# Optimization experiments

Measured on AMD Instinct MI355X. Metric: run time of the kernel, lower is better.

Reference implementation:

```python
import jax, jax.numpy as jnp
import numpy as np

EMBED_DIM = 256
HEADS = 8
HEAD_DIM = EMBED_DIM // HEADS
T = 8            # time grid points
N0, N1 = 32, 32  # spatial grid
MAX_PATCH = 16   # static slot budget per cell (last slot = grid latent token)
NEG = -1e30


def construct_grid():
    g0 = jnp.linspace(0.0, 1.0, N0)
    g1 = jnp.linspace(0.0, 1.0, N1)
    G0, G1 = jnp.meshgrid(g0, g1, indexing='ij')
    return jnp.stack([G0, G1], axis=-1)  # [N0, N1, 2]


def setup_inputs() -> dict:
    key = jax.random.key(0)
    ks = jax.random.split(key, 8)
    m, n = 4, 16384
    x = jax.random.uniform(ks[0], (m, n, 3))                       # coords: (time, s0, s1) in [0,1]
    z = jax.random.normal(ks[1], (m, n, EMBED_DIM))
    time_grid = jnp.tile(jnp.linspace(0.0, 1.0, T)[None], (m, 1))  # [m, T] uniform time grid
    latents = jax.random.normal(ks[2], (N0, N1, EMBED_DIM))
    grid = construct_grid()
    s = 1.0 / np.sqrt(EMBED_DIM)
    Wq = jax.random.normal(ks[3], (EMBED_DIM, EMBED_DIM)) * s
    Wk = jax.random.normal(ks[4], (EMBED_DIM, EMBED_DIM)) * s
    Wv = jax.random.normal(ks[5], (EMBED_DIM, EMBED_DIM)) * s
    Wo = jax.random.normal(ks[6], (EMBED_DIM, EMBED_DIM)) * s
    return {'x': x, 'z': z, 'time_grid': time_grid, 'latents': latents,
            'grid': grid, 'Wq': Wq, 'Wk': Wk, 'Wv': Wv, 'Wo': Wo}


def _cumcount(idx):
    # idx: [n] int; returns per-element count of prior occurrences of the same value
    n = idx.shape[0]
    order = jnp.argsort(idx)                 # stable
    srt = idx[order]
    ar = jnp.arange(n)
    is_start = jnp.concatenate([jnp.array([True]), srt[1:] != srt[:-1]])
    seg_start = jax.lax.cummax(jnp.where(is_start, ar, 0), axis=0)
    cc = ar - seg_start
    return jnp.zeros_like(idx).at[order].set(cc.astype(idx.dtype))


def _forward(x, z, time_grid, latents, grid, Wq, Wk, Wv, Wo):
    m, n, _ = x.shape
    t = time_grid.shape[1]
    S = t * N0 * N1
    # --- build x_grid: repeat spatial grid over (m,t), insert time coord at dim 0 ---
    xg_sp = jnp.broadcast_to(grid[None, None], (m, t, N0, N1, 2))
    tg = jnp.broadcast_to(time_grid[:, :, None, None, None], (m, t, N0, N1, 1))
    x_grid = jnp.concatenate([tg, xg_sp], axis=-1)          # [m,t,N0,N1,3]
    # --- nearest gridded neighbour (k=1): per-dim rounding on the regular grid ---
    grid_shape = jnp.array([t, N0, N1], jnp.float32)
    xg_flat = x_grid.reshape(m, S, 3)
    xmin = xg_flat.min(axis=1)                               # [m,3]
    xmax = xg_flat.max(axis=1)
    spacing = (xmax - xmin) / (grid_shape - 1.0)             # [m,3]
    multi = jnp.floor((x - xmin[:, None] + spacing[:, None] / 2) / spacing[:, None])
    multi = jnp.clip(multi, 0.0, grid_shape - 1.0)
    strides = jnp.array([N0 * N1, N1, 1], jnp.float32)
    nearest = jnp.sum(multi * strides, axis=-1).astype(jnp.int32)  # [m,n] flat cell id
    # --- per-cell slot allocation via cumulative count ---
    cum = jax.vmap(_cumcount)(nearest)                       # [m,n]
    P = MAX_PATCH
    valid = cum < (P - 1)                                    # last slot reserved for grid token
    bidx = jnp.arange(m)[:, None]
    cell = jnp.where(valid, nearest, S)                      # out-of-bounds -> dropped
    slot = jnp.minimum(cum, P - 2)
    # --- scatter points into the joint grid [m, S, P, E]; slot P-1 = grid latent ---
    joint = jnp.zeros((m, S, P, EMBED_DIM), z.dtype)
    joint = joint.at[bidx, cell, slot].set(z, mode='drop')
    z_grid_flat = jnp.broadcast_to(
        latents.reshape(1, 1, N0 * N1, EMBED_DIM), (m, t, N0 * N1, EMBED_DIM)
    ).reshape(m, S, EMBED_DIM)
    joint = joint.at[:, :, P - 1].set(z_grid_flat)
    counts = jnp.zeros((m, S), jnp.int32).at[bidx, cell].add(1, mode='drop')
    counts = jnp.minimum(counts, P - 1)
    att_mask = jnp.concatenate(
        [jnp.arange(P - 1)[None, None] < counts[..., None],
         jnp.ones((m, S, 1), bool)], axis=-1)                # [m,S,P]
    # --- masked multi-head cross attention: 1 query (grid latent) per cell ---
    q = (z_grid_flat @ Wq).reshape(m, S, HEADS, HEAD_DIM)
    k = (joint @ Wk).reshape(m, S, P, HEADS, HEAD_DIM)
    v = (joint @ Wv).reshape(m, S, P, HEADS, HEAD_DIM)
    logits = jnp.einsum('mshd,msphd->mshp', q, k) / np.sqrt(HEAD_DIM)
    logits = jnp.where(att_mask[:, :, None, :], logits, NEG)
    attn = jax.nn.softmax(logits, axis=-1)
    out = jnp.einsum('mshp,msphd->mshd', attn, v).reshape(m, S, EMBED_DIM) @ Wo
    z_grid = out.reshape(m, t, N0, N1, EMBED_DIM)
    return x_grid, z_grid


def reference(x, z, time_grid, latents, grid, Wq, Wk, Wv, Wo):
    return _forward(x, z, time_grid, latents, grid, Wq, Wk, Wv, Wo)
```

## Files before the change

### kernel.cpp

```cpp
#include <hip/hip_runtime.h>
#include <hip/hip_bf16.h>

#define T_ 8
#define N0_ 32
#define N1_ 32
#define SP_ (N0_*N1_)
#define S_ (T_*SP_)
#define E_ 256
#define P_ 16
#define NH_ 8
#define HD_ 32

typedef __attribute__((ext_vector_type(8))) short short8;
typedef __attribute__((ext_vector_type(4))) float f32x4;
typedef __attribute__((ext_vector_type(8))) unsigned short u16x8;

__device__ __forceinline__ unsigned short f2bf(float f) {
  __hip_bfloat16 h = __float2bfloat16(f);
  return *reinterpret_cast<unsigned short*>(&h);
}
__device__ __forceinline__ float bf2f(unsigned short u) {
  return __uint_as_float((unsigned)u << 16);
}

__device__ __forceinline__ void gl_lds16(const void* g, void* l) {
  __builtin_amdgcn_global_load_lds(
      (const __attribute__((address_space(1))) unsigned int*)(g),
      (__attribute__((address_space(3))) unsigned int*)(l), 16, 0, 0);
}

__global__ __launch_bounds__(256) void prep(const float* __restrict__ x,
                                            const float* __restrict__ tg,
                                            const float* __restrict__ grid,
                                            float* __restrict__ out,
                                            int* __restrict__ counts,
                                            int* __restrict__ cell_raw,
                                            const float* __restrict__ Wq,
                                            const float* __restrict__ Wk,
                                            const float* __restrict__ Wv,
                                            const float* __restrict__ Wo,
                                            unsigned short* __restrict__ wT,
                                            int m, int n, int tot_xg) {
  __shared__ float ts[64][65];
  __shared__ float st[4][6];
  int bid = blockIdx.x;
  int tid = threadIdx.x;
  if (bid < 256) {
    if (tid < 64) {
      float mn0 = 1e30f, mx0 = -1e30f, mn1 = 1e30f, mx1 = -1e30f;
      for (int i = tid; i < SP_; i += 64) {
        float g0 = grid[i*2], g1 = grid[i*2+1];
        mn0 = fminf(mn0, g0); mx0 = fmaxf(mx0, g0);
        mn1 = fminf(mn1, g1); mx1 = fmaxf(mx1, g1);
      }
      for (int msk = 32; msk; msk >>= 1) {
        mn0 = fminf(mn0, __shfl_xor(mn0, msk));
        mx0 = fmaxf(mx0, __shfl_xor(mx0, msk));
        mn1 = fminf(mn1, __shfl_xor(mn1, msk));
        mx1 = fmaxf(mx1, __shfl_xor(mx1, msk));
      }
      if (tid == 0) {
        for (int b = 0; b < m; ++b) {
          float tmn = 1e30f, tmx = -1e30f;
          for (int tt = 0; tt < T_; ++tt) {
            float v = tg[b*T_ + tt];
            tmn = fminf(tmn, v); tmx = fmaxf(tmx, v);
          }
          st[b][0] = tmn; st[b][1] = mn0; st[b][2] = mn1;
          st[b][3] = (tmx - tmn) / (float)(T_ - 1);
          st[b][4] = (mx0 - mn0) / (float)(N0_ - 1);
          st[b][5] = (mx1 - mn1) / (float)(N1_ - 1);
        }
      }
    }
    __syncthreads();
    int idx = bid * 256 + tid;
    if (idx < tot_xg) {
      int sp = idx & (SP_ - 1);
      int bt = idx >> 10;
      out[idx*3 + 0] = tg[bt];
      out[idx*3 + 1] = grid[sp*2 + 0];
      out[idx*3 + 2] = grid[sp*2 + 1];
    }
    if (idx < m*n) {
      int b = idx / n;
      int j = idx - b*n;
      const float* s = st[b];
      float xt = x[(size_t)idx*3 + 0], x0 = x[(size_t)idx*3 + 1], x1 = x[(size_t)idx*3 + 2];
      float m0 = floorf((xt - s[0] + s[3]*0.5f) / s[3]);
      float m1 = floorf((x0 - s[1] + s[4]*0.5f) / s[4]);
      float m2 = floorf((x1 - s[2] + s[5]*0.5f) / s[5]);
      m0 = fminf(fmaxf(m0, 0.f), (float)(T_ - 1));
      m1 = fminf(fmaxf(m1, 0.f), (float)(N0_ - 1));
      m2 = fminf(fmaxf(m2, 0.f), (float)(N1_ - 1));
      int sc = (int)m0 * SP_ + (int)m1 * N1_ + (int)m2;
      int cg = b * S_ + sc;
      int old = atomicAdd(&counts[cg], 1);
      if (old < P_) cell_raw[(size_t)cg * P_ + old] = j;
    }
    return;
  }
  int wb = bid - 256;
  int mat = wb >> 4;
  int tile = wb & 15;
  int tr = (tile >> 2) * 64;
  int tc = (tile & 3) * 64;
  const float* W = mat == 0 ? Wq : mat == 1 ? Wk : mat == 2 ? Wv : Wo;
  int r = tid >> 2, c0 = (tid & 3) * 16;
#pragma unroll
  for (int i = 0; i < 4; ++i) {
    float4 v = *(const float4*)&W[(size_t)(tr + r) * 256 + tc + c0 + i*4];
    ts[r][c0 + i*4 + 0] = v.x; ts[r][c0 + i*4 + 1] = v.y;
    ts[r][c0 + i*4 + 2] = v.z; ts[r][c0 + i*4 + 3] = v.w;
  }
  __syncthreads();
  u16x8 o0, o1;
#pragma unroll
  for (int i = 0; i < 8; ++i) o0[i] = f2bf(ts[c0 + i][r]);
#pragma unroll
  for (int i = 0; i < 8; ++i) o1[i] = f2bf(ts[c0 + 8 + i][r]);
  unsigned short* dst = wT + (size_t)(mat * 256 + tc + r) * 256 + tr + c0;
  *(u16x8*)dst = o0;
  *(u16x8*)(dst + 8) = o1;
}

template <typename OutT>
__device__ __forceinline__ void f32a_body(char* __restrict__ ldsbuf,
                                          const float* __restrict__ A,
                                          const unsigned short* __restrict__ BT,
                                          OutT* __restrict__ C,
                                          int CP, int ldc, int L, int tid) {
  float* As = (float*)ldsbuf;
  unsigned short* Bs = (unsigned short*)(ldsbuf + 32768);
  int rp = L / CP, cp = L - rp * CP;

  int wid = tid >> 6, lane = tid & 63, l15 = lane & 15, slot = lane >> 4;
  int wr = (wid >> 1) * 64, wc = (wid & 1) * 64;

  int arl = lane >> 4, aG = lane & 15;
  int brl = lane >> 3, bG = lane & 7;

  f32x4 acc[4][4] = {};

#pragma unroll
  for (int kt = 0; kt < 4; ++kt) {
#pragma unroll
    for (int d = 0; d < 8; ++d) {
      int row = wid * 32 + d * 4 + arl;
      const float* src = A + (size_t)(rp * 128 + row) * 256 + kt * 64
                         + (size_t)((aG ^ (row & 15)) << 2);
      gl_lds16(src, As + (wid * 32 + d * 4) * 64);
    }
#pragma unroll
    for (int d = 0; d < 4; ++d) {
      int row = wid * 32 + d * 8 + brl;
      const unsigned short* src = BT + (size_t)(cp * 128 + row) * 256 + kt * 64
                                  + (size_t)((bG ^ (row & 7)) << 3);
      gl_lds16(src, Bs + (wid * 32 + d * 8) * 64);
    }
    asm volatile("s_waitcnt vmcnt(0)" ::: "memory");
    __builtin_amdgcn_s_barrier();
    asm volatile("" ::: "memory");
#pragma unroll
    for (int kf = 0; kf < 2; ++kf) {
      short8 afr[4], bfr[4];
      int kg = kf * 4 + slot;
#pragma unroll
      for (int mm = 0; mm < 4; ++mm) {
        int row = wr + mm * 16 + l15;
        f32x4 a0 = *(const f32x4*)&As[row * 64 + (((2 * kg    ) ^ l15) << 2)];
        f32x4 a1 = *(const f32x4*)&As[row * 64 + (((2 * kg + 1) ^ l15) << 2)];
        short8 af;
        af[0]=f2bf(a0[0]); af[1]=f2bf(a0[1]); af[2]=f2bf(a0[2]); af[3]=f2bf(a0[3]);
        af[4]=f2bf(a1[0]); af[5]=f2bf(a1[1]); af[6]=f2bf(a1[2]); af[7]=f2bf(a1[3]);
        afr[mm] = af;
      }
#pragma unroll
      for (int nn = 0; nn < 4; ++nn) {
        int col = wc + nn * 16 + l15;
        bfr[nn] = *(const short8*)&Bs[col * 64 + ((kg ^ (l15 & 7)) << 3)];
      }
#pragma unroll
      for (int mm = 0; mm < 4; ++mm)
#pragma unroll
        for (int nn = 0; nn < 4; ++nn)
          acc[mm][nn] = __builtin_amdgcn_mfma_f32_16x16x32_bf16(afr[mm], bfr[nn], acc[mm][nn], 0, 0, 0);
    }
    asm volatile("" ::: "memory");
    __builtin_amdgcn_s_barrier();
    asm volatile("" ::: "memory");
  }

#pragma unroll
  for (int mm = 0; mm < 4; ++mm) {
#pragma unroll
    for (int nn = 0; nn < 4; ++nn) {
      int grow0 = rp * 128 + wr + mm * 16 + slot * 4;
      int gcol  = cp * 128 + wc + nn * 16 + l15;
#pragma unroll
      for (int j = 0; j < 4; ++j) {
        size_t o = (size_t)(grow0 + j) * ldc + gcol;
        if constexpr (__is_same(OutT, float)) C[o] = acc[mm][nn][j];
        else                                  C[o] = __float2bfloat16(acc[mm][nn][j]);
      }
    }
  }
}

template <typename OutT>
__device__ __forceinline__ void g2l_body(unsigned short* __restrict__ ldsbuf,
                                         const unsigned short* __restrict__ A,
                                         const unsigned short* __restrict__ BT,
                                         OutT* __restrict__ C,
                                         int CP, int ldc, int L, int tid) {
  int rp = L / CP, cp = L - rp * CP;

  int wid = tid >> 6, lane = tid & 63, l15 = lane & 15, slot = lane >> 4;
  int wr = (wid >> 1) * 64, wc = (wid & 1) * 64;

  int r8 = lane >> 3, k8 = lane & 7;
  int colsw = (k8 ^ r8) << 3;
  const unsigned short* ga0 = A  + (size_t)(rp * 128 + wid * 32 + r8) * 256 + colsw;
  const unsigned short* gb0 = BT + (size_t)(cp * 128 + wid * 32 + r8) * 256 + colsw;
  unsigned short* As = ldsbuf;
  unsigned short* Bs = ldsbuf + 8192;

  f32x4 acc[4][4] = {};

#pragma unroll
  for (int kt = 0; kt < 4; ++kt) {
    const unsigned short* ga = ga0 + kt * 64;
    const unsigned short* gb = gb0 + kt * 64;
    gl_lds16(ga,          As + (wid*32     ) * 64);
    gl_lds16(ga +  8*256, As + (wid*32 +  8) * 64);
    gl_lds16(ga + 16*256, As + (wid*32 + 16) * 64);
    gl_lds16(ga + 24*256, As + (wid*32 + 24) * 64);
    gl_lds16(gb,          Bs + (wid*32     ) * 64);
    gl_lds16(gb +  8*256, Bs + (wid*32 +  8) * 64);
    gl_lds16(gb + 16*256, Bs + (wid*32 + 16) * 64);
    gl_lds16(gb + 24*256, Bs + (wid*32 + 24) * 64);
    asm volatile("s_waitcnt vmcnt(0)" ::: "memory");
    __builtin_amdgcn_s_barrier();
    asm volatile("" ::: "memory");
#pragma unroll
    for (int kf = 0; kf < 2; ++kf) {
      short8 afr[4], bfr[4];
      int sx = (kf * 4 + slot) ^ (l15 & 7);
#pragma unroll
      for (int mm = 0; mm < 4; ++mm) {
        int row = wr + mm * 16 + l15;
        afr[mm] = *(const short8*)&As[row * 64 + (sx << 3)];
      }
#pragma unroll
      for (int nn = 0; nn < 4; ++nn) {
        int col = wc + nn * 16 + l15;
        bfr[nn] = *(const short8*)&Bs[col * 64 + (sx << 3)];
      }
#pragma unroll
      for (int mm = 0; mm < 4; ++mm)
#pragma unroll
        for (int nn = 0; nn < 4; ++nn)
          acc[mm][nn] = __builtin_amdgcn_mfma_f32_16x16x32_bf16(afr[mm], bfr[nn], acc[mm][nn], 0, 0, 0);
    }
    asm volatile("" ::: "memory");
    __builtin_amdgcn_s_barrier();
    asm volatile("" ::: "memory");
  }

#pragma unroll
  for (int mm = 0; mm < 4; ++mm) {
#pragma unroll
    for (int nn = 0; nn < 4; ++nn) {
      int grow0 = rp * 128 + wr + mm * 16 + slot * 4;
      int gcol  = cp * 128 + wc + nn * 16 + l15;
#pragma unroll
      for (int j = 0; j < 4; ++j) {
        size_t o = (size_t)(grow0 + j) * ldc + gcol;
        if constexpr (__is_same(OutT, float)) C[o] = acc[mm][nn][j];
        else                                  C[o] = __float2bfloat16(acc[mm][nn][j]);
      }
    }
  }
}

__global__ __launch_bounds__(256, 3) void phase2(const float* __restrict__ z,
                                                 const unsigned short* __restrict__ wT,
                                                 __hip_bfloat16* __restrict__ kv,
                                                 const float* __restrict__ latents,
                                                 float* __restrict__ lat,
                                                 const int* __restrict__ counts,
                                                 int* __restrict__ cell_raw,
                                                 int* __restrict__ pts2, int total) {
  __shared__ char lds[49152];
  int bid = blockIdx.x;
  if (bid < 2048) {
    int L = (bid & 7) * 256 + (bid >> 3);
    f32a_body<__hip_bfloat16>(lds, z, wT + (size_t)256*256, kv, 4, 512, L, threadIdx.x);
    return;
  }
  if (bid < 2096) {
    f32a_body<float>(lds, latents, wT, lat, 6, 768, bid - 2048, threadIdx.x);
    return;
  }
  int cg = (bid - 2096) * 256 + threadIdx.x;
  if (cg >= total) return;
  int cnt = counts[cg];
  int stored = cnt < P_ ? cnt : P_;
  int eff = cnt < (P_ - 1) ? cnt : (P_ - 1);
  int* p = cell_raw + (size_t)cg * P_;
  for (int i = 1; i < stored; ++i) {
    int key = p[i]; int j = i - 1;
    while (j >= 0 && p[j] > key) { p[j+1] = p[j]; --j; }
    p[j+1] = key;
  }
  int* o = pts2 + (size_t)cg * P_;
  o[0] = eff;
  for (int i = 0; i < eff; ++i) o[1 + i] = p[i];
}

template <typename OutT>
__global__ __launch_bounds__(256, 3) void gemm_g2l(const unsigned short* __restrict__ A,
                                                   const unsigned short* __restrict__ BT,
                                                   OutT* __restrict__ C,
                                                   int CP, int ldc) {
  __shared__ unsigned short lds[2 * 128 * 64];
  int nb = gridDim.x, bid = blockIdx.x;
  int L = bid;
  if ((nb & 7) == 0) L = (bid & 7) * (nb >> 3) + (bid >> 3);
  g2l_body<OutT>(lds, A, BT, C, CP, ldc, L, threadIdx.x);
}

__global__ __launch_bounds__(256) void attn_kernel(
    const float* __restrict__ lat,
    const __hip_bfloat16* __restrict__ kv,
    const int* __restrict__ pts2,
    __hip_bfloat16* __restrict__ attn_out, int n) {
  const float scale = 0.17677669529663687f;
  int wid = threadIdx.x >> 6;
  int lane = threadIdx.x & 63;
  int cellg = blockIdx.x * 4 + wid;
  int b = cellg >> 13;
  int c = cellg & (SP_ - 1);
  int d0 = lane << 2;

  const int* pp = pts2 + (size_t)cellg * P_;
  int4 h0 = *(const int4*)pp;
  int eff = h0.x;

  const float* latc = lat + c * 768 + d0;
  float4 q  = *(const float4*)latc;
  float4 kl = *(const float4*)(latc + 256);
  float4 vl = *(const float4*)(latc + 512);

  float p15 = q.x*kl.x + q.y*kl.y + q.z*kl.z + q.w*kl.w;
  p15 += __shfl_xor(p15, 1);
  p15 += __shfl_xor(p15, 2);
  p15 += __shfl_xor(p15, 4);
  float e15 = __expf(p15 * scale);
  float ssum = e15;
  float4 acc;
  acc.x = e15 * vl.x; acc.y = e15 * vl.y; acc.z = e15 * vl.z; acc.w = e15 * vl.w;

  const unsigned short* kvp = (const unsigned short*)kv;
  size_t bbase = (size_t)b * n;

  int pt[4]; pt[0] = h0.y; pt[1] = h0.z; pt[2] = h0.w; pt[3] = 0;
  int done = 0, cap = 3;
  while (done < eff) {
    int np = eff - done; if (np > cap) np = cap;
    ushort4 kr[4], vr[4];
#pragma unroll
    for (int i = 0; i < 4; ++i) if (i < np) {
      size_t row = (bbase + (size_t)pt[i]) * 512;
      kr[i] = *(const ushort4*)(kvp + row + d0);
      vr[i] = *(const ushort4*)(kvp + row + 256 + d0);
    }
    float e[4];
#pragma unroll
    for (int i = 0; i < 4; ++i) if (i < np) {
      float p = q.x*bf2f(kr[i].x) + q.y*bf2f(kr[i].y) + q.z*bf2f(kr[i].z) + q.w*bf2f(kr[i].w);
      p += __shfl_xor(p, 1);
      p += __shfl_xor(p, 2);
      p += __shfl_xor(p, 4);
      e[i] = __expf(p * scale);
    }
#pragma unroll
    for (int i = 0; i < 4; ++i) if (i < np) {
      ssum += e[i];
      acc.x += e[i] * bf2f(vr[i].x);
      acc.y += e[i] * bf2f(vr[i].y);
      acc.z += e[i] * bf2f(vr[i].z);
      acc.w += e[i] * bf2f(vr[i].w);
    }
    done += np;
    cap = 4;
    if (done < eff) {
      int4 h = *(const int4*)(pp + 1 + done);
      pt[0] = h.x; pt[1] = h.y; pt[2] = h.z; pt[3] = h.w;
    }
  }
  float inv = 1.f / ssum;
  ushort4 o;
  o.x = f2bf(acc.x * inv); o.y = f2bf(acc.y * inv);
  o.z = f2bf(acc.z * inv); o.w = f2bf(acc.w * inv);
  *(ushort4*)((unsigned short*)attn_out + (size_t)cellg * E_ + d0) = o;
}

extern "C" void kernel_launch(void* const* d_in, const int* in_sizes, int n_in,
                              void* d_out, int out_size, void* d_ws, size_t ws_size,
                              hipStream_t stream) {
  const float* x       = (const float*)d_in[0];
  const float* z       = (const float*)d_in[1];
  const float* tg      = (const float*)d_in[2];
  const float* latents = (const float*)d_in[3];
  const float* grid    = (const float*)d_in[4];
  const float* Wq      = (const float*)d_in[5];
  const float* Wk      = (const float*)d_in[6];
  const float* Wv      = (const float*)d_in[7];
  const float* Wo      = (const float*)d_in[8];

  int m = in_sizes[2] / T_;
  int n = in_sizes[1] / (m * E_);
  int MS = m * S_;
  float* out = (float*)d_out;
  int tot_xg = m * T_ * SP_;

  char* w = (char*)d_ws;
  auto alloc = [&](size_t bytes) { char* p = w; w += (bytes + 255) & ~(size_t)255; return p; };
  int*   counts     = (int*)  alloc((size_t)MS * 4);
  int*   cell_raw   = (int*)  alloc((size_t)MS * P_ * 4);
  int*   pts2       = (int*)  alloc((size_t)MS * P_ * 4);
  unsigned short* wT = (unsigned short*)alloc((size_t)1024 * 256 * 2);
  float* lat        = (float*)alloc((size_t)SP_ * 768 * 4);
  __hip_bfloat16* kv       = (__hip_bfloat16*)alloc((size_t)m * n * 512 * 2);
  __hip_bfloat16* attn_out = (__hip_bfloat16*)alloc((size_t)MS * E_ * 2);

  (void)hipMemsetAsync(counts, 0, (size_t)MS * 4, stream);

  prep<<<320, 256, 0, stream>>>(x, tg, grid, out, counts, cell_raw,
                                Wq, Wk, Wv, Wo, wT, m, n, tot_xg);

  phase2<<<2224, 256, 0, stream>>>(z, wT, kv, latents, lat, counts, cell_raw, pts2, MS);

  attn_kernel<<<MS/4, 256, 0, stream>>>(lat, kv, pts2, attn_out, n);

  gemm_g2l<float><<<512, 256, 0, stream>>>(
      (const unsigned short*)attn_out, wT + (size_t)768*256, out + (size_t)tot_xg * 3, 2, 256);
}
```

Measured before the change: 83.46 us.

## Defer V projection past attention and fuse V/O projections into attention kernel

Only K is projected for all points now. The attention kernel accumulates softmax-weighted raw z rows per head and applies Wv afterwards on the per-cell mixed vectors, since attn·(zWv) = (attn·z)Wv. The V and Wo projections are then done with MFMA inside the same kernel, which removes the separate output GEMM and the attn_out round trip. This halves the large point projection GEMM and the kv buffer. In exchange it adds per-head fp32 z gathers, eight heads of accumulator registers per lane, and small per-block GEMMs whose weights are read straight from global memory.

```diff
diff --git a/kernel.cpp b/kernel.cpp
--- a/kernel.cpp
+++ b/kernel.cpp
@@ -207,85 +207,9 @@
   }
 }
 
-template <typename OutT>
-__device__ __forceinline__ void g2l_body(unsigned short* __restrict__ ldsbuf,
-                                         const unsigned short* __restrict__ A,
-                                         const unsigned short* __restrict__ BT,
-                                         OutT* __restrict__ C,
-                                         int CP, int ldc, int L, int tid) {
-  int rp = L / CP, cp = L - rp * CP;
-
-  int wid = tid >> 6, lane = tid & 63, l15 = lane & 15, slot = lane >> 4;
-  int wr = (wid >> 1) * 64, wc = (wid & 1) * 64;
-
-  int r8 = lane >> 3, k8 = lane & 7;
-  int colsw = (k8 ^ r8) << 3;
-  const unsigned short* ga0 = A  + (size_t)(rp * 128 + wid * 32 + r8) * 256 + colsw;
-  const unsigned short* gb0 = BT + (size_t)(cp * 128 + wid * 32 + r8) * 256 + colsw;
-  unsigned short* As = ldsbuf;
-  unsigned short* Bs = ldsbuf + 8192;
-
-  f32x4 acc[4][4] = {};
-
-#pragma unroll
-  for (int kt = 0; kt < 4; ++kt) {
-    const unsigned short* ga = ga0 + kt * 64;
-    const unsigned short* gb = gb0 + kt * 64;
-    gl_lds16(ga,          As + (wid*32     ) * 64);
-    gl_lds16(ga +  8*256, As + (wid*32 +  8) * 64);
-    gl_lds16(ga + 16*256, As + (wid*32 + 16) * 64);
-    gl_lds16(ga + 24*256, As + (wid*32 + 24) * 64);
-    gl_lds16(gb,          Bs + (wid*32     ) * 64);
-    gl_lds16(gb +  8*256, Bs + (wid*32 +  8) * 64);
-    gl_lds16(gb + 16*256, Bs + (wid*32 + 16) * 64);
-    gl_lds16(gb + 24*256, Bs + (wid*32 + 24) * 64);
-    asm volatile("s_waitcnt vmcnt(0)" ::: "memory");
-    __builtin_amdgcn_s_barrier();
-    asm volatile("" ::: "memory");
-#pragma unroll
-    for (int kf = 0; kf < 2; ++kf) {
-      short8 afr[4], bfr[4];
-      int sx = (kf * 4 + slot) ^ (l15 & 7);
-#pragma unroll
-      for (int mm = 0; mm < 4; ++mm) {
-        int row = wr + mm * 16 + l15;
-        afr[mm] = *(const short8*)&As[row * 64 + (sx << 3)];
-      }
-#pragma unroll
-      for (int nn = 0; nn < 4; ++nn) {
-        int col = wc + nn * 16 + l15;
-        bfr[nn] = *(const short8*)&Bs[col * 64 + (sx << 3)];
-      }
-#pragma unroll
-      for (int mm = 0; mm < 4; ++mm)
-#pragma unroll
-        for (int nn = 0; nn < 4; ++nn)
-          acc[mm][nn] = __builtin_amdgcn_mfma_f32_16x16x32_bf16(afr[mm], bfr[nn], acc[mm][nn], 0, 0, 0);
-    }
-    asm volatile("" ::: "memory");
-    __builtin_amdgcn_s_barrier();
-    asm volatile("" ::: "memory");
-  }
-
-#pragma unroll
-  for (int mm = 0; mm < 4; ++mm) {
-#pragma unroll
-    for (int nn = 0; nn < 4; ++nn) {
-      int grow0 = rp * 128 + wr + mm * 16 + slot * 4;
-      int gcol  = cp * 128 + wc + nn * 16 + l15;
-#pragma unroll
-      for (int j = 0; j < 4; ++j) {
-        size_t o = (size_t)(grow0 + j) * ldc + gcol;
-        if constexpr (__is_same(OutT, float)) C[o] = acc[mm][nn][j];
-        else                                  C[o] = __float2bfloat16(acc[mm][nn][j]);
-      }
-    }
-  }
-}
-
 __global__ __launch_bounds__(256, 3) void phase2(const float* __restrict__ z,
                                                  const unsigned short* __restrict__ wT,
-                                                 __hip_bfloat16* __restrict__ kv,
+                                                 __hip_bfloat16* __restrict__ k16,
                                                  const float* __restrict__ latents,
                                                  float* __restrict__ lat,
                                                  const int* __restrict__ counts,
@@ -293,16 +217,16 @@
                                                  int* __restrict__ pts2, int total) {
   __shared__ char lds[49152];
   int bid = blockIdx.x;
-  if (bid < 2048) {
-    int L = (bid & 7) * 256 + (bid >> 3);
-    f32a_body<__hip_bfloat16>(lds, z, wT + (size_t)256*256, kv, 4, 512, L, threadIdx.x);
+  if (bid < 1024) {
+    int L = (bid & 7) * 128 + (bid >> 3);
+    f32a_body<__hip_bfloat16>(lds, z, wT + (size_t)256*256, k16, 2, 256, L, threadIdx.x);
     return;
   }
-  if (bid < 2096) {
-    f32a_body<float>(lds, latents, wT, lat, 6, 768, bid - 2048, threadIdx.x);
+  if (bid < 1072) {
+    f32a_body<float>(lds, latents, wT, lat, 6, 768, bid - 1024, threadIdx.x);
     return;
   }
-  int cg = (bid - 2096) * 256 + threadIdx.x;
+  int cg = (bid - 1072) * 256 + threadIdx.x;
   if (cg >= total) return;
   int cnt = counts[cg];
   int stored = cnt < P_ ? cnt : P_;
@@ -318,92 +242,139 @@
   for (int i = 0; i < eff; ++i) o[1 + i] = p[i];
 }
 
-template <typename OutT>
-__global__ __launch_bounds__(256, 3) void gemm_g2l(const unsigned short* __restrict__ A,
-                                                   const unsigned short* __restrict__ BT,
-                                                   OutT* __restrict__ C,
-                                                   int CP, int ldc) {
-  __shared__ unsigned short lds[2 * 128 * 64];
-  int nb = gridDim.x, bid = blockIdx.x;
-  int L = bid;
-  if ((nb & 7) == 0) L = (bid & 7) * (nb >> 3) + (bid >> 3);
-  g2l_body<OutT>(lds, A, BT, C, CP, ldc, L, threadIdx.x);
-}
-
-__global__ __launch_bounds__(256) void attn_kernel(
-    const float* __restrict__ lat,
-    const __hip_bfloat16* __restrict__ kv,
-    const int* __restrict__ pts2,
-    __hip_bfloat16* __restrict__ attn_out, int n) {
+__global__ __launch_bounds__(256, 2) void mega_attn(const float* __restrict__ z,
+                                                    const float* __restrict__ latents,
+                                                    const float* __restrict__ lat,
+                                                    const __hip_bfloat16* __restrict__ k16,
+                                                    const unsigned short* __restrict__ wTv,
+                                                    const unsigned short* __restrict__ wTo,
+                                                    const int* __restrict__ pts2,
+                                                    float* __restrict__ outZ, int n) {
+  __shared__ unsigned short mixlds[16 * 2048];
+  __shared__ unsigned short avlds[16 * 256];
   const float scale = 0.17677669529663687f;
-  int wid = threadIdx.x >> 6;
-  int lane = threadIdx.x & 63;
-  int cellg = blockIdx.x * 4 + wid;
-  int b = cellg >> 13;
-  int c = cellg & (SP_ - 1);
+  int tid = threadIdx.x, w = tid >> 6, lane = tid & 63;
   int d0 = lane << 2;
-
-  const int* pp = pts2 + (size_t)cellg * P_;
-  int4 h0 = *(const int4*)pp;
-  int eff = h0.x;
-
-  const float* latc = lat + c * 768 + d0;
-  float4 q  = *(const float4*)latc;
-  float4 kl = *(const float4*)(latc + 256);
-  float4 vl = *(const float4*)(latc + 512);
-
-  float p15 = q.x*kl.x + q.y*kl.y + q.z*kl.z + q.w*kl.w;
-  p15 += __shfl_xor(p15, 1);
-  p15 += __shfl_xor(p15, 2);
-  p15 += __shfl_xor(p15, 4);
-  float e15 = __expf(p15 * scale);
-  float ssum = e15;
-  float4 acc;
-  acc.x = e15 * vl.x; acc.y = e15 * vl.y; acc.z = e15 * vl.z; acc.w = e15 * vl.w;
-
-  const unsigned short* kvp = (const unsigned short*)kv;
-  size_t bbase = (size_t)b * n;
-
-  int pt[4]; pt[0] = h0.y; pt[1] = h0.z; pt[2] = h0.w; pt[3] = 0;
-  int done = 0, cap = 3;
-  while (done < eff) {
-    int np = eff - done; if (np > cap) np = cap;
-    ushort4 kr[4], vr[4];
-#pragma unroll
-    for (int i = 0; i < 4; ++i) if (i < np) {
-      size_t row = (bbase + (size_t)pt[i]) * 512;
-      kr[i] = *(const ushort4*)(kvp + row + d0);
-      vr[i] = *(const ushort4*)(kvp + row + 256 + d0);
-    }
-    float e[4];
-#pragma unroll
-    for (int i = 0; i < 4; ++i) if (i < np) {
-      float p = q.x*bf2f(kr[i].x) + q.y*bf2f(kr[i].y) + q.z*bf2f(kr[i].z) + q.w*bf2f(kr[i].w);
-      p += __shfl_xor(p, 1);
-      p += __shfl_xor(p, 2);
-      p += __shfl_xor(p, 4);
-      e[i] = __expf(p * scale);
-    }
-#pragma unroll
-    for (int i = 0; i < 4; ++i) if (i < np) {
-      ssum += e[i];
-      acc.x += e[i] * bf2f(vr[i].x);
-      acc.y += e[i] * bf2f(vr[i].y);
-      acc.z += e[i] * bf2f(vr[i].z);
-      acc.w += e[i] * bf2f(vr[i].w);
-    }
-    done += np;
-    cap = 4;
-    if (done < eff) {
-      int4 h = *(const int4*)(pp + 1 + done);
-      pt[0] = h.x; pt[1] = h.y; pt[2] = h.z; pt[3] = h.w;
-    }
-  }
-  float inv = 1.f / ssum;
-  ushort4 o;
-  o.x = f2bf(acc.x * inv); o.y = f2bf(acc.y * inv);
-  o.z = f2bf(acc.z * inv); o.w = f2bf(acc.w * inv);
-  *(ushort4*)((unsigned short*)attn_out + (size_t)cellg * E_ + d0) = o;
+  int l7 = lane & 7;
+  int cg0 = blockIdx.x * 16;
+
+  for (int cc = 0; cc < 4; ++cc) {
+    int cellL = w * 4 + cc;
+    int cellg = cg0 + cellL;
+    int bidx = cellg >> 13;
+    int c = cellg & (SP_ - 1);
+
+    const float* latc = lat + c * 768 + d0;
+    float4 q  = *(const float4*)latc;
+    float4 kl = *(const float4*)(latc + 256);
+
+    const int* pp = pts2 + (size_t)cellg * P_;
+    int4 h0 = *(const int4*)pp;
+    int eff = h0.x;
+
+    float ss[8];
+    float mx[8][4];
+    {
+      float p = q.x*kl.x + q.y*kl.y + q.z*kl.z + q.w*kl.w;
+      p += __shfl_xor(p, 1); p += __shfl_xor(p, 2); p += __shfl_xor(p, 4);
+      float e = __expf(p * scale);
+      float4 zl = *(const float4*)(latents + (size_t)c * 256 + d0);
+#pragma unroll
+      for (int h = 0; h < 8; ++h) {
+        float eh = __shfl(e, (h << 3) | l7);
+        ss[h] = eh;
+        mx[h][0] = eh*zl.x; mx[h][1] = eh*zl.y; mx[h][2] = eh*zl.z; mx[h][3] = eh*zl.w;
+      }
+    }
+    size_t bb = (size_t)bidx * n;
+    const unsigned short* kp = (const unsigned short*)k16;
+    int pt[4]; pt[0] = h0.y; pt[1] = h0.z; pt[2] = h0.w; pt[3] = 0;
+    int done = 0, cap = 3;
+    while (done < eff) {
+      int np = eff - done; if (np > cap) np = cap;
+      ushort4 kr[4]; float4 zr[4];
+#pragma unroll
+      for (int i = 0; i < 4; ++i) if (i < np) {
+        size_t row = bb + (size_t)pt[i];
+        kr[i] = *(const ushort4*)(kp + row * 256 + d0);
+        zr[i] = *(const float4*)(z + row * 256 + d0);
+      }
+#pragma unroll
+      for (int i = 0; i < 4; ++i) if (i < np) {
+        float p = q.x*bf2f(kr[i].x) + q.y*bf2f(kr[i].y) + q.z*bf2f(kr[i].z) + q.w*bf2f(kr[i].w);
+        p += __shfl_xor(p, 1); p += __shfl_xor(p, 2); p += __shfl_xor(p, 4);
+        float e = __expf(p * scale);
+#pragma unroll
+        for (int h = 0; h < 8; ++h) {
+          float eh = __shfl(e, (h << 3) | l7);
+          ss[h] += eh;
+          mx[h][0] += eh*zr[i].x; mx[h][1] += eh*zr[i].y;
+          mx[h][2] += eh*zr[i].z; mx[h][3] += eh*zr[i].w;
+        }
+      }
+      done += np;
+      cap = 4;
+      if (done < eff) {
+        int4 hh = *(const int4*)(pp + 1 + done);
+        pt[0] = hh.x; pt[1] = hh.y; pt[2] = hh.z; pt[3] = hh.w;
+      }
+    }
+    unsigned base = (unsigned)cellL * 4096;
+    unsigned K = cellL & 7;
+#pragma unroll
+    for (int h = 0; h < 8; ++h) {
+      float inv = 1.f / ss[h];
+      unsigned g = (unsigned)(h * 32 + (lane >> 1));
+      unsigned addr = base + ((g ^ K) << 4) + ((unsigned)(d0 & 7) << 1);
+      ushort4 v;
+      v.x = f2bf(mx[h][0] * inv); v.y = f2bf(mx[h][1] * inv);
+      v.z = f2bf(mx[h][2] * inv); v.w = f2bf(mx[h][3] * inv);
+      *(ushort4*)((char*)mixlds + addr) = v;
+    }
+  }
+  __syncthreads();
+
+  int l15 = lane & 15, slot = lane >> 4;
+#pragma unroll
+  for (int hh = 0; hh < 2; ++hh) {
+    int h = w + hh * 4;
+    f32x4 acc0 = {}, acc1 = {};
+#pragma unroll
+    for (int ks = 0; ks < 8; ++ks) {
+      unsigned gA = (unsigned)(h * 32 + ks * 4 + slot);
+      short8 afr = *(const short8*)((const char*)mixlds + l15 * 4096 + ((gA ^ (unsigned)(l15 & 7)) << 4));
+      short8 b0 = *(const short8*)(wTv + (size_t)(h * 32 + l15) * 256 + ks * 32 + slot * 8);
+      short8 b1 = *(const short8*)(wTv + (size_t)(h * 32 + 16 + l15) * 256 + ks * 32 + slot * 8);
+      acc0 = __builtin_amdgcn_mfma_f32_16x16x32_bf16(afr, b0, acc0, 0, 0, 0);
+      acc1 = __builtin_amdgcn_mfma_f32_16x16x32_bf16(afr, b1, acc1, 0, 0, 0);
+    }
+#pragma unroll
+    for (int j = 0; j < 4; ++j) {
+      unsigned row = (unsigned)(slot * 4 + j);
+      unsigned c0 = (unsigned)(h * 32 + l15);
+      unsigned c1 = (unsigned)(h * 32 + 16 + l15);
+      *(unsigned short*)((char*)avlds + row * 512 + (((c0 >> 3) ^ row) << 4) + ((c0 & 7) << 1)) = f2bf(acc0[j]);
+      *(unsigned short*)((char*)avlds + row * 512 + (((c1 >> 3) ^ row) << 4) + ((c1 & 7) << 1)) = f2bf(acc1[j]);
+    }
+  }
+  __syncthreads();
+
+  f32x4 oacc[4] = {};
+#pragma unroll
+  for (int ks = 0; ks < 8; ++ks) {
+    unsigned gA = (unsigned)(ks * 4 + slot);
+    short8 afr = *(const short8*)((const char*)avlds + l15 * 512 + ((gA ^ (unsigned)l15) << 4));
+#pragma unroll
+    for (int nn = 0; nn < 4; ++nn) {
+      short8 bf = *(const short8*)(wTo + (size_t)(w * 64 + nn * 16 + l15) * 256 + ks * 32 + slot * 8);
+      oacc[nn] = __builtin_amdgcn_mfma_f32_16x16x32_bf16(afr, bf, oacc[nn], 0, 0, 0);
+    }
+  }
+#pragma unroll
+  for (int nn = 0; nn < 4; ++nn)
+#pragma unroll
+    for (int j = 0; j < 4; ++j)
+      outZ[(size_t)(cg0 + slot * 4 + j) * 256 + w * 64 + nn * 16 + l15] = oacc[nn][j];
 }
 
 extern "C" void kernel_launch(void* const* d_in, const int* in_sizes, int n_in,
@@ -432,18 +403,16 @@
   int*   pts2       = (int*)  alloc((size_t)MS * P_ * 4);
   unsigned short* wT = (unsigned short*)alloc((size_t)1024 * 256 * 2);
   float* lat        = (float*)alloc((size_t)SP_ * 768 * 4);
-  __hip_bfloat16* kv       = (__hip_bfloat16*)alloc((size_t)m * n * 512 * 2);
-  __hip_bfloat16* attn_out = (__hip_bfloat16*)alloc((size_t)MS * E_ * 2);
+  __hip_bfloat16* k16 = (__hip_bfloat16*)alloc((size_t)m * n * 256 * 2);
 
   (void)hipMemsetAsync(counts, 0, (size_t)MS * 4, stream);
 
   prep<<<320, 256, 0, stream>>>(x, tg, grid, out, counts, cell_raw,
                                 Wq, Wk, Wv, Wo, wT, m, n, tot_xg);
 
-  phase2<<<2224, 256, 0, stream>>>(z, wT, kv, latents, lat, counts, cell_raw, pts2, MS);
-
-  attn_kernel<<<MS/4, 256, 0, stream>>>(lat, kv, pts2, attn_out, n);
-
-  gemm_g2l<float><<<512, 256, 0, stream>>>(
-      (const unsigned short*)attn_out, wT + (size_t)768*256, out + (size_t)tot_xg * 3, 2, 256);
-}
+  phase2<<<1200, 256, 0, stream>>>(z, wT, k16, latents, lat, counts, cell_raw, pts2, MS);
+
+  mega_attn<<<MS/16, 256, 0, stream>>>(z, latents, lat, k16,
+                                       wT + (size_t)2*256*256, wT + (size_t)3*256*256,
+                                       pts2, out + (size_t)tot_xg * 3, n);
+}
```

Result: slower. 143.1 us (+71.4%).
